# Kernel optimization log

Hardware: AMD Instinct MI355X
Metric: run time of the kernel (lower is better)

The kernel has to match this reference:

```python
import jax, jax.numpy as jnp
import numpy as np

HIDDEN = 2048
B, T, K = 64, 512, 49  # K = 7x7 spatial grid

def setup_inputs() -> dict:
    key = jax.random.key(0)
    ks = jax.random.split(key, 7)
    def xavier(k, shape):
        fan_in, fan_out = shape[1], shape[0]
        bound = float(np.sqrt(6.0 / (fan_in + fan_out)))
        return jax.random.uniform(k, shape, jnp.float32, -bound, bound)
    return {
        "V": jax.random.normal(ks[0], (B, K, HIDDEN), jnp.float32),
        "h_t": jax.random.normal(ks[1], (B, T, HIDDEN), jnp.float32),
        "sent_t": jax.random.normal(ks[2], (B, T, HIDDEN), jnp.float32),
        "Wv": xavier(ks[3], (K, HIDDEN)),
        "Wg": xavier(ks[4], (K, HIDDEN)),
        "Ws": xavier(ks[5], (K, HIDDEN)),
        "Wh": xavier(ks[6], (1, K)),
    }

def reference(V, h_t, sent_t, Wv, Wg, Ws, Wh):
    # Dropout is identity (eval mode / deterministic reference).
    wh = Wh[0]                                    # [K]
    pv = jnp.einsum('bkd,jd->bkj', V, Wv)         # [B,K,K]
    pg = jnp.einsum('btd,jd->btj', h_t, Wg)       # [B,T,K]
    content_v = pv[:, None, :, :] + pg[:, :, None, :]   # [B,T,K,K]
    z_t = jnp.tanh(content_v) @ wh                # [B,T,K]
    alpha_t = jax.nn.softmax(z_t, axis=-1)        # spatial attention
    c_t = jnp.einsum('btk,bkd->btd', alpha_t, V)  # [B,T,HIDDEN]
    content_s = jnp.einsum('btd,jd->btj', sent_t, Ws) + pg  # [B,T,K]
    z_ext = jnp.tanh(content_s) @ wh              # [B,T]
    extend = jnp.concatenate([z_t, z_ext[..., None]], axis=-1)  # [B,T,K+1]
    alpha_hat = jax.nn.softmax(extend, axis=-1)
    beta_t = alpha_hat[:, :, -1:]                 # sentinel gate [B,T,1]
    c_hat_t = beta_t * sent_t + (1.0 - beta_t) * c_t
    return (c_hat_t, alpha_t, beta_t)
```

## Files before the change

### kernel.cpp

```cpp
#include <hip/hip_runtime.h>

#define HIDDEN 2048
#define NB 64
#define NT 512
#define NK 49

#define BM 128
#define BK 64
#define NCH (HIDDEN/BK)

typedef __attribute__((ext_vector_type(4))) float f32x4;
typedef __attribute__((ext_vector_type(8))) short short8;

__device__ __forceinline__ unsigned cvtpk_bf16(float a, float b) {
    unsigned r;
    asm("v_cvt_pk_bf16_f32 %0, %1, %2" : "=v"(r) : "v"(a), "v"(b));
    return r;
}

__device__ __forceinline__ unsigned short f2bf(float x) {
    union { float f; unsigned u; } v; v.f = x;
    unsigned r = v.u + 0x7FFF + ((v.u >> 16) & 1);
    return (unsigned short)(r >> 16);
}

__global__ __launch_bounds__(256) void convert_w(
    const float* __restrict__ Wg, const float* __restrict__ Ws,
    const float* __restrict__ Wv, unsigned short* __restrict__ Wf)
{
    int tau = blockIdx.x * 256 + threadIdx.x;
    int m   = tau >> 14;
    int rem = tau & 16383;
    int st  = rem >> 8;
    int c   = (rem >> 6) & 3;
    int l   = rem & 63;
    int col = c * 16 + (l & 15);
    int k0  = st * 32 + ((l >> 4) << 3);

    const float* W = (m == 0) ? Wg : (m == 1) ? Ws : Wv;
    unsigned short out[8];
    if (col < NK) {
        const float* p = W + (size_t)col * HIDDEN + k0;
        #pragma unroll
        for (int j = 0; j < 8; j++) out[j] = f2bf(p[j]);
    } else {
        #pragma unroll
        for (int j = 0; j < 8; j++) out[j] = 0;
    }
    unsigned short* dst = Wf + (size_t)tau * 8;
    #pragma unroll
    for (int j = 0; j < 8; j++) dst[j] = out[j];
}

__global__ __launch_bounds__(512) void gemm_mfma(
    const float* __restrict__ h, const float* __restrict__ s,
    const float* __restrict__ V, const unsigned short* __restrict__ Wf,
    float* __restrict__ pg, float* __restrict__ ps, float* __restrict__ pv)
{
    int tid = threadIdx.x;
    int w = tid >> 6, lane = tid & 63;
    int blk = blockIdx.x;

    const float* A; float* C; int rowBase; const unsigned short* wfm; int Mrows;
    if (blk < 256)      { A = h; C = pg; rowBase = blk * BM;         wfm = Wf;                       Mrows = 32768; }
    else if (blk < 512) { A = s; C = ps; rowBase = (blk - 256) * BM; wfm = Wf + (size_t)16384 * 8;   Mrows = 32768; }
    else                { A = V; C = pv; rowBase = (blk - 512) * BM; wfm = Wf + (size_t)32768 * 8;   Mrows = 3136;  }

    __shared__ float  Alds[2][BM * BK];
    __shared__ short8 Blds[2][512];

    const short8* wfp = (const short8*)wfm;
    int rt0 = w * 16;

    f32x4 acc0 = {0.f, 0.f, 0.f, 0.f};
    f32x4 acc1 = acc0, acc2 = acc0, acc3 = acc0;

#define DMA_AB(ch, buf) { \
    _Pragma("unroll") \
    for (int i = 0; i < 4; i++) { \
        int rt = rt0 + i * 4 + (lane >> 4); \
        int gr = rowBase + rt; if (gr > Mrows - 1) gr = Mrows - 1; \
        int sg = (lane & 15) ^ (rt & 7); \
        const float* src = A + (size_t)gr * HIDDEN + (ch) * BK + sg * 4; \
        __builtin_amdgcn_global_load_lds((const void*)src, \
            (void*)&Alds[buf][(rt0 + i * 4) * BK], 16, 0, 0); \
    } \
    { const short8* srcb = wfp + (size_t)((ch) * 8 + w) * 64 + lane; \
      __builtin_amdgcn_global_load_lds((const void*)srcb, \
          (void*)&Blds[buf][w * 64], 16, 0, 0); } }

#define CHUNK_COMPUTE(buf) { \
    const float*  al = &Alds[buf][0]; \
    const short8* bl = &Blds[buf][0]; \
    int rr = lane & 15; \
    int row = rt0 + rr; \
    _Pragma("unroll") \
    for (int st = 0; st < 2; st++) { \
        int cs = st * 8 + ((lane >> 4) << 1); \
        float4 f0 = *(const float4*)&al[row * BK + ((cs    ) ^ (rr & 7)) * 4]; \
        float4 f1 = *(const float4*)&al[row * BK + ((cs + 1) ^ (rr & 7)) * 4]; \
        union { short8 v; unsigned u[4]; } a_; \
        a_.u[0] = cvtpk_bf16(f0.x, f0.y); \
        a_.u[1] = cvtpk_bf16(f0.z, f0.w); \
        a_.u[2] = cvtpk_bf16(f1.x, f1.y); \
        a_.u[3] = cvtpk_bf16(f1.z, f1.w); \
        short8 b0 = bl[(st * 4 + 0) * 64 + lane]; \
        short8 b1 = bl[(st * 4 + 1) * 64 + lane]; \
        short8 b2 = bl[(st * 4 + 2) * 64 + lane]; \
        short8 b3 = bl[(st * 4 + 3) * 64 + lane]; \
        acc0 = __builtin_amdgcn_mfma_f32_16x16x32_bf16(a_.v, b0, acc0, 0, 0, 0); \
        acc1 = __builtin_amdgcn_mfma_f32_16x16x32_bf16(a_.v, b1, acc1, 0, 0, 0); \
        acc2 = __builtin_amdgcn_mfma_f32_16x16x32_bf16(a_.v, b2, acc2, 0, 0, 0); \
        acc3 = __builtin_amdgcn_mfma_f32_16x16x32_bf16(a_.v, b3, acc3, 0, 0, 0); \
    } }

    DMA_AB(0, 0)

    #pragma unroll 1
    for (int ch = 0; ch < NCH; ch++) {
        int cur = ch & 1;
        __syncthreads();
        if (ch + 1 < NCH) { DMA_AB(ch + 1, cur ^ 1) }
        CHUNK_COMPUTE(cur)
    }

#undef DMA_AB
#undef CHUNK_COMPUTE

    int colb  = lane & 15;
    int rquad = (lane >> 4) << 2;
    int rowb  = rowBase + rt0 + rquad;
    float* crow = C + (size_t)rowb * NK + colb;
    #pragma unroll
    for (int r = 0; r < 4; r++) {
        if (rowb + r < Mrows) {
            crow[(size_t)r * NK + 0]  = acc0[r];
            crow[(size_t)r * NK + 16] = acc1[r];
            crow[(size_t)r * NK + 32] = acc2[r];
            if (colb == 0) crow[(size_t)r * NK + 48] = acc3[r];
        }
    }
}

__device__ __forceinline__ float ftanh(float x) {
    float e = __expf(2.f * x);
    return 1.f - 2.f * __builtin_amdgcn_rcpf(e + 1.f);
}

__global__ __launch_bounds__(256) void zab_kernel(
    const float* __restrict__ pg, const float* __restrict__ ps,
    const float* __restrict__ pv, const float* __restrict__ Wh,
    float* __restrict__ alpha, float* __restrict__ beta)
{
    int w = threadIdx.x >> 6, lane = threadIdx.x & 63;
    int row = blockIdx.x * 4 + w;
    int b = row >> 9;

    const float* pgrow = pg + (size_t)row * NK;
    const float* psrow = ps + (size_t)row * NK;

    float va = 0.f;
    if (lane < NK)
        va = ftanh(psrow[lane] + pgrow[lane]) * Wh[lane];
    float z_ext = va;
    #pragma unroll
    for (int off = 32; off; off >>= 1) z_ext += __shfl_xor(z_ext, off);

    float z = -1e30f;
    if (lane < NK) {
        const float* pvrow = pv + ((size_t)b * NK + lane) * NK;
        float acc = 0.f;
        for (int j = 0; j < NK; j++)
            acc = fmaf(ftanh(pvrow[j] + pgrow[j]), Wh[j], acc);
        z = acc;
    }

    float m = z;
    #pragma unroll
    for (int off = 32; off; off >>= 1) m = fmaxf(m, __shfl_xor(m, off));
    float p = (lane < NK) ? __expf(z - m) : 0.f;
    float ssum = p;
    #pragma unroll
    for (int off = 32; off; off >>= 1) ssum += __shfl_xor(ssum, off);
    float a = p * __builtin_amdgcn_rcpf(ssum);

    if (lane < NK)
        alpha[(size_t)row * NK + lane] = a;

    float me = fmaxf(m, z_ext);
    float se = ssum * __expf(m - me) + __expf(z_ext - me);
    float bet = __expf(z_ext - me) * __builtin_amdgcn_rcpf(se);
    if (lane == 0) beta[row] = bet;
}

__global__ __launch_bounds__(256) void chat_kernel(
    const float* __restrict__ V, const float* __restrict__ sent,
    const float* __restrict__ alpha, const float* __restrict__ beta,
    float* __restrict__ chat)
{
    int d0 = blockIdx.x * 128;
    int t0 = blockIdx.y * 32;
    int b  = blockIdx.z;

    __shared__ float alpha_s[NK][36];
    __shared__ float beta_s[32];

    int tid = threadIdx.x;

    const float* arow = alpha + ((size_t)b * NT + t0) * NK;
    for (int i = tid; i < 32 * NK; i += 256) {
        int t = i / NK, k = i - t * NK;
        alpha_s[k][t] = arow[i];
    }
    if (tid < 32) beta_s[tid] = beta[(size_t)b * NT + t0 + tid];
    __syncthreads();

    int tx = tid & 31;
    int ty = tid >> 5;

    const float* vp = V + (size_t)b * NK * HIDDEN + d0 + tx * 4;

    float4 acc[4];
    #pragma unroll
    for (int i = 0; i < 4; i++) acc[i] = make_float4(0.f, 0.f, 0.f, 0.f);

    #pragma unroll 7
    for (int k = 0; k < NK; k++) {
        float4 vv = *(const float4*)(vp + (size_t)k * HIDDEN);
        float4 a4 = *(const float4*)&alpha_s[k][ty * 4];
        acc[0].x = fmaf(a4.x, vv.x, acc[0].x);
        acc[0].y = fmaf(a4.x, vv.y, acc[0].y);
        acc[0].z = fmaf(a4.x, vv.z, acc[0].z);
        acc[0].w = fmaf(a4.x, vv.w, acc[0].w);
        acc[1].x = fmaf(a4.y, vv.x, acc[1].x);
        acc[1].y = fmaf(a4.y, vv.y, acc[1].y);
        acc[1].z = fmaf(a4.y, vv.z, acc[1].z);
        acc[1].w = fmaf(a4.y, vv.w, acc[1].w);
        acc[2].x = fmaf(a4.z, vv.x, acc[2].x);
        acc[2].y = fmaf(a4.z, vv.y, acc[2].y);
        acc[2].z = fmaf(a4.z, vv.z, acc[2].z);
        acc[2].w = fmaf(a4.z, vv.w, acc[2].w);
        acc[3].x = fmaf(a4.w, vv.x, acc[3].x);
        acc[3].y = fmaf(a4.w, vv.y, acc[3].y);
        acc[3].z = fmaf(a4.w, vv.z, acc[3].z);
        acc[3].w = fmaf(a4.w, vv.w, acc[3].w);
    }

    #pragma unroll
    for (int i = 0; i < 4; i++) {
        int t = ty * 4 + i;
        float bt = beta_s[t];
        const float* sp = sent + ((size_t)b * NT + t0 + t) * HIDDEN + d0 + tx * 4;
        float*       op = chat + ((size_t)b * NT + t0 + t) * HIDDEN + d0 + tx * 4;
        float4 sv = *(const float4*)sp;
        float4 o;
        o.x = fmaf(bt, sv.x, (1.f - bt) * acc[i].x);
        o.y = fmaf(bt, sv.y, (1.f - bt) * acc[i].y);
        o.z = fmaf(bt, sv.z, (1.f - bt) * acc[i].z);
        o.w = fmaf(bt, sv.w, (1.f - bt) * acc[i].w);
        *(float4*)op = o;
    }
}

extern "C" void kernel_launch(void* const* d_in, const int* in_sizes, int n_in,
                              void* d_out, int out_size, void* d_ws, size_t ws_size,
                              hipStream_t stream)
{
    const float* V    = (const float*)d_in[0];
    const float* h_t  = (const float*)d_in[1];
    const float* sent = (const float*)d_in[2];
    const float* Wv   = (const float*)d_in[3];
    const float* Wg   = (const float*)d_in[4];
    const float* Ws   = (const float*)d_in[5];
    const float* Wh   = (const float*)d_in[6];

    float* out   = (float*)d_out;
    float* chat  = out;
    float* alpha = out + (size_t)NB * NT * HIDDEN;
    float* beta  = alpha + (size_t)NB * NT * NK;

    float* ws = (float*)d_ws;
    float* pg = ws;
    float* ps = pg + (size_t)NB * NT * NK;
    float* pv = ps + (size_t)NB * NT * NK;
    unsigned short* Wf = (unsigned short*)(pv + (size_t)NB * NK * NK);

    convert_w<<<192, 256, 0, stream>>>(Wg, Ws, Wv, Wf);
    gemm_mfma<<<537, 512, 0, stream>>>(h_t, sent, V, Wf, pg, ps, pv);
    zab_kernel<<<(NB * NT) / 4, 256, 0, stream>>>(pg, ps, pv, Wh, alpha, beta);
    chat_kernel<<<dim3(HIDDEN / 128, NT / 32, NB), 256, 0, stream>>>(V, sent, alpha, beta, chat);
}
```

Before: 358.3 us.

## Retile GEMM to 64-row blocks and read bf16 weights directly from global

The projection GEMM now uses 64-row by 128-deep tiles with 256-thread blocks, which doubles the grid to 1073 blocks. The weight operand is no longer staged through LDS via DMA; each wave reads the pre-packed bf16 weight fragments straight from global memory (cache-resident) inside the compute loop. The aims are to cut barrier count per K, shrink LDS use for better occupancy, and drop the B staging traffic. The risk is global-load latency exposed inside the MFMA loop, since the weight loads are no longer prefetched.

```diff
diff --git a/kernel.cpp b/kernel.cpp
--- a/kernel.cpp
+++ b/kernel.cpp
@@ -5,8 +5,8 @@
 #define NT 512
 #define NK 49
 
-#define BM 128
-#define BK 64
+#define BM 64
+#define BK 128
 #define NCH (HIDDEN/BK)
 
 typedef __attribute__((ext_vector_type(4))) float f32x4;
@@ -52,7 +52,7 @@
     for (int j = 0; j < 8; j++) dst[j] = out[j];
 }
 
-__global__ __launch_bounds__(512) void gemm_mfma(
+__global__ __launch_bounds__(256) void gemm_mfma(
     const float* __restrict__ h, const float* __restrict__ s,
     const float* __restrict__ V, const unsigned short* __restrict__ Wf,
     float* __restrict__ pg, float* __restrict__ ps, float* __restrict__ pv)
@@ -62,12 +62,11 @@
     int blk = blockIdx.x;
 
     const float* A; float* C; int rowBase; const unsigned short* wfm; int Mrows;
-    if (blk < 256)      { A = h; C = pg; rowBase = blk * BM;         wfm = Wf;                       Mrows = 32768; }
-    else if (blk < 512) { A = s; C = ps; rowBase = (blk - 256) * BM; wfm = Wf + (size_t)16384 * 8;   Mrows = 32768; }
-    else                { A = V; C = pv; rowBase = (blk - 512) * BM; wfm = Wf + (size_t)32768 * 8;   Mrows = 3136;  }
-
-    __shared__ float  Alds[2][BM * BK];
-    __shared__ short8 Blds[2][512];
+    if (blk < 512)       { A = h; C = pg; rowBase = blk * BM;          wfm = Wf;                     Mrows = 32768; }
+    else if (blk < 1024) { A = s; C = ps; rowBase = (blk - 512) * BM;  wfm = Wf + (size_t)16384 * 8; Mrows = 32768; }
+    else                 { A = V; C = pv; rowBase = (blk - 1024) * BM; wfm = Wf + (size_t)32768 * 8; Mrows = 3136;  }
+
+    __shared__ float Alds[2][BM * BK];
 
     const short8* wfp = (const short8*)wfm;
     int rt0 = w * 16;
@@ -75,56 +74,53 @@
     f32x4 acc0 = {0.f, 0.f, 0.f, 0.f};
     f32x4 acc1 = acc0, acc2 = acc0, acc3 = acc0;
 
-#define DMA_AB(ch, buf) { \
+#define DMA_A(ch, buf) { \
     _Pragma("unroll") \
-    for (int i = 0; i < 4; i++) { \
-        int rt = rt0 + i * 4 + (lane >> 4); \
-        int gr = rowBase + rt; if (gr > Mrows - 1) gr = Mrows - 1; \
-        int sg = (lane & 15) ^ (rt & 7); \
-        const float* src = A + (size_t)gr * HIDDEN + (ch) * BK + sg * 4; \
+    for (int i = 0; i < 8; i++) { \
+        int lr = rt0 + i * 2 + (lane >> 5); \
+        int gr = rowBase + lr; if (gr > Mrows - 1) gr = Mrows - 1; \
+        int sp = (lane & 31) ^ (lr & 7); \
+        const float* src = A + (size_t)gr * HIDDEN + (ch) * BK + sp * 4; \
         __builtin_amdgcn_global_load_lds((const void*)src, \
-            (void*)&Alds[buf][(rt0 + i * 4) * BK], 16, 0, 0); \
-    } \
-    { const short8* srcb = wfp + (size_t)((ch) * 8 + w) * 64 + lane; \
-      __builtin_amdgcn_global_load_lds((const void*)srcb, \
-          (void*)&Blds[buf][w * 64], 16, 0, 0); } }
-
-#define CHUNK_COMPUTE(buf) { \
-    const float*  al = &Alds[buf][0]; \
-    const short8* bl = &Blds[buf][0]; \
-    int rr = lane & 15; \
-    int row = rt0 + rr; \
+            (void*)&Alds[buf][(rt0 + i * 2) * BK], 16, 0, 0); \
+    } }
+
+#define CHUNK_COMPUTE(ch, buf) { \
+    const float* al = &Alds[buf][0]; \
+    int row = rt0 + (lane & 15); \
+    int g2 = (lane >> 4) << 1; \
     _Pragma("unroll") \
-    for (int st = 0; st < 2; st++) { \
-        int cs = st * 8 + ((lane >> 4) << 1); \
-        float4 f0 = *(const float4*)&al[row * BK + ((cs    ) ^ (rr & 7)) * 4]; \
-        float4 f1 = *(const float4*)&al[row * BK + ((cs + 1) ^ (rr & 7)) * 4]; \
+    for (int st = 0; st < 4; st++) { \
+        int d = st * 8 + g2; \
+        float4 f0 = *(const float4*)&al[row * BK + ((d    ) ^ (row & 7)) * 4]; \
+        float4 f1 = *(const float4*)&al[row * BK + ((d + 1) ^ (row & 7)) * 4]; \
         union { short8 v; unsigned u[4]; } a_; \
         a_.u[0] = cvtpk_bf16(f0.x, f0.y); \
         a_.u[1] = cvtpk_bf16(f0.z, f0.w); \
         a_.u[2] = cvtpk_bf16(f1.x, f1.y); \
         a_.u[3] = cvtpk_bf16(f1.z, f1.w); \
-        short8 b0 = bl[(st * 4 + 0) * 64 + lane]; \
-        short8 b1 = bl[(st * 4 + 1) * 64 + lane]; \
-        short8 b2 = bl[(st * 4 + 2) * 64 + lane]; \
-        short8 b3 = bl[(st * 4 + 3) * 64 + lane]; \
+        int gst = (ch) * 4 + st; \
+        short8 b0 = wfp[(size_t)(gst * 4 + 0) * 64 + lane]; \
+        short8 b1 = wfp[(size_t)(gst * 4 + 1) * 64 + lane]; \
+        short8 b2 = wfp[(size_t)(gst * 4 + 2) * 64 + lane]; \
+        short8 b3 = wfp[(size_t)(gst * 4 + 3) * 64 + lane]; \
         acc0 = __builtin_amdgcn_mfma_f32_16x16x32_bf16(a_.v, b0, acc0, 0, 0, 0); \
         acc1 = __builtin_amdgcn_mfma_f32_16x16x32_bf16(a_.v, b1, acc1, 0, 0, 0); \
         acc2 = __builtin_amdgcn_mfma_f32_16x16x32_bf16(a_.v, b2, acc2, 0, 0, 0); \
         acc3 = __builtin_amdgcn_mfma_f32_16x16x32_bf16(a_.v, b3, acc3, 0, 0, 0); \
     } }
 
-    DMA_AB(0, 0)
+    DMA_A(0, 0)
 
     #pragma unroll 1
     for (int ch = 0; ch < NCH; ch++) {
         int cur = ch & 1;
         __syncthreads();
-        if (ch + 1 < NCH) { DMA_AB(ch + 1, cur ^ 1) }
-        CHUNK_COMPUTE(cur)
-    }
-
-#undef DMA_AB
+        if (ch + 1 < NCH) { DMA_A(ch + 1, cur ^ 1) }
+        CHUNK_COMPUTE(ch, cur)
+    }
+
+#undef DMA_A
 #undef CHUNK_COMPUTE
 
     int colb  = lane & 15;
@@ -286,7 +282,7 @@
     unsigned short* Wf = (unsigned short*)(pv + (size_t)NB * NK * NK);
 
     convert_w<<<192, 256, 0, stream>>>(Wg, Ws, Wv, Wf);
-    gemm_mfma<<<537, 512, 0, stream>>>(h_t, sent, V, Wf, pg, ps, pv);
+    gemm_mfma<<<1073, 256, 0, stream>>>(h_t, sent, V, Wf, pg, ps, pv);
     zab_kernel<<<(NB * NT) / 4, 256, 0, stream>>>(pg, ps, pv, Wh, alpha, beta);
     chat_kernel<<<dim3(HIDDEN / 128, NT / 32, NB), 256, 0, stream>>>(V, sent, alpha, beta, chat);
 }
```

After: 372.2 us. 1.04x slower.
